# Optimization experiments

Hardware: AMD Instinct MI355X
Metric: run time of the kernel (lower is better)

Reference implementation:

```python
import jax, jax.numpy as jnp
import numpy as np

N = 50000      # nodes
E = 800000     # edges
D_IN = 512     # input feature dim
H1, C1 = 8, 8  # conv1: heads, per-head channels -> 64 concat
D_MID = H1 * C1
D_OUT = 64     # output_dim (classes)


def _lin(key, din, dout):
    # torch.nn.Linear default init: U(-1/sqrt(din), 1/sqrt(din))
    kw, kb = jax.random.split(key)
    s = 1.0 / np.sqrt(din)
    W = jax.random.uniform(kw, (din, dout), minval=-s, maxval=s, dtype=jnp.float32)
    b = jax.random.uniform(kb, (dout,), minval=-s, maxval=s, dtype=jnp.float32)
    return W, b


def setup_inputs() -> dict:
    key = jax.random.key(0)
    ks = jax.random.split(key, 10)
    x = jax.random.normal(ks[0], (N, D_IN), dtype=jnp.float32)
    edge_index = jax.random.randint(ks[1], (2, E), 0, N, dtype=jnp.int64)
    Wq1, bq1 = _lin(ks[2], D_IN, D_MID)
    Wk1, bk1 = _lin(ks[3], D_IN, D_MID)
    Wv1, bv1 = _lin(ks[4], D_IN, D_MID)
    Ws1, bs1 = _lin(ks[5], D_IN, D_MID)          # skip (concat=True -> heads*out)
    Wq2, bq2 = _lin(ks[6], D_MID, D_OUT)
    Wk2, bk2 = _lin(ks[7], D_MID, D_OUT)
    Wv2, bv2 = _lin(ks[8], D_MID, D_OUT)
    Ws2, bs2 = _lin(ks[9], D_MID, D_OUT)         # skip (concat=False -> out)
    return dict(x=x, edge_index=edge_index,
                Wq1=Wq1, bq1=bq1, Wk1=Wk1, bk1=bk1, Wv1=Wv1, bv1=bv1, Ws1=Ws1, bs1=bs1,
                Wq2=Wq2, bq2=bq2, Wk2=Wk2, bk2=bk2, Wv2=Wv2, bv2=bv2, Ws2=Ws2, bs2=bs2)


def transformer_conv(x, src, dst, Wq, bq, Wk, bk, Wv, bv, Ws, bs, heads, out_ch, concat):
    # PyG TransformerConv (edge_dim=None, beta=False, root_weight=True), eval mode
    n = x.shape[0]
    q = (x @ Wq + bq).reshape(n, heads, out_ch)
    k = (x @ Wk + bk).reshape(n, heads, out_ch)
    v = (x @ Wv + bv).reshape(n, heads, out_ch)
    # per-edge scaled dot-product attention logits [E, H]
    alpha = jnp.einsum('ehc,ehc->eh', q[dst], k[src]) / np.sqrt(out_ch)
    # scatter-softmax over incoming edges of each target node
    amax = jax.ops.segment_max(alpha, dst, num_segments=n)            # [N, H]
    ex = jnp.exp(alpha - amax[dst])
    denom = jax.ops.segment_sum(ex, dst, num_segments=n)              # [N, H]
    a = ex / (denom[dst] + 1e-16)                                     # [E, H]
    # weighted scatter-add of values
    out = jax.ops.segment_sum(a[:, :, None] * v[src], dst, num_segments=n)  # [N, H, C]
    out = out.reshape(n, heads * out_ch) if concat else out.mean(axis=1)
    return out + (x @ Ws + bs)  # root/skip connection


def reference(x, edge_index, Wq1, bq1, Wk1, bk1, Wv1, bv1, Ws1, bs1,
              Wq2, bq2, Wk2, bk2, Wv2, bv2, Ws2, bs2):
    src, dst = edge_index[0], edge_index[1]   # message flows j=src -> i=dst
    # dropout layers are no-ops in eval mode
    h = transformer_conv(x, src, dst, Wq1, bq1, Wk1, bk1, Wv1, bv1, Ws1, bs1, H1, C1, True)
    h = jax.nn.elu(h)
    h = transformer_conv(h, src, dst, Wq2, bq2, Wk2, bk2, Wv2, bv2, Ws2, bs2, 1, D_OUT, False)
    return jax.nn.log_softmax(h, axis=-1)
```

## Files before the change

kernel.cpp:

```cpp
#include <hip/hip_runtime.h>
#include <hip/hip_bf16.h>
#include <math.h>


typedef __attribute__((ext_vector_type(4))) float f32x4;
typedef __attribute__((ext_vector_type(8))) short bf16x8;
typedef __attribute__((ext_vector_type(8))) unsigned short u16x8;

__device__ inline unsigned short f2bf(float f) {
    union { float f; unsigned u; } v; v.f = f;
    unsigned r = (v.u + 0x7fffu + ((v.u >> 16) & 1u)) >> 16;
    return (unsigned short)r;
}
__device__ inline float bf2f(unsigned short u) {
    union { unsigned u; float f; } v; v.u = ((unsigned)u) << 16; return v.f;
}

#define NEGBIG (-1e30f)

__device__ inline void prep_panel(int i, int K,
                                  const float* __restrict__ W0, const float* __restrict__ b0,
                                  const float* __restrict__ W1, const float* __restrict__ b1,
                                  const float* __restrict__ W2, const float* __restrict__ b2,
                                  const float* __restrict__ W3, const float* __restrict__ b3,
                                  unsigned short* __restrict__ Btp, float* __restrict__ bias) {
    int tot = 4 * K * 64;
    if (i < tot) {
        int j    = i & 7;
        int lane = (i >> 3) & 63;
        int ni   = (i >> 9) & 3;
        int kk   = (i >> 11) & 1;
        int w    = (i >> 12) & 3;
        int ks   = i >> 14;
        int ncol = ni * 16 + (lane & 15);
        int k    = ks * 64 + kk * 32 + ((lane >> 4) << 3) + j;
        const float* W = (w == 0) ? W0 : (w == 1) ? W1 : (w == 2) ? W2 : W3;
        Btp[i] = f2bf(W[k * 64 + ncol]);
    }
    if (i < 256) {
        int which = i >> 6;
        const float* b = (which == 0) ? b0 : (which == 1) ? b1 : (which == 2) ? b2 : b3;
        bias[i] = b[i & 63];
    }
}

__global__ void setup_all(const float* __restrict__ Wq1, const float* __restrict__ bq1,
                          const float* __restrict__ Wk1, const float* __restrict__ bk1,
                          const float* __restrict__ Wv1, const float* __restrict__ bv1,
                          const float* __restrict__ Ws1, const float* __restrict__ bs1,
                          const float* __restrict__ Wq2, const float* __restrict__ bq2,
                          const float* __restrict__ Wk2, const float* __restrict__ bk2,
                          const float* __restrict__ Wv2, const float* __restrict__ bv2,
                          const float* __restrict__ Ws2, const float* __restrict__ bs2,
                          unsigned short* __restrict__ bt1, float* __restrict__ bias1,
                          unsigned short* __restrict__ bt2, float* __restrict__ bias2,
                          int* __restrict__ deg, int* __restrict__ cursor, int N) {
    const int b = blockIdx.x;
    const int tid = threadIdx.x;
    if (b < 512) {
        prep_panel(b * 256 + tid, 512, Wq1, bq1, Wk1, bk1, Wv1, bv1, Ws1, bs1, bt1, bias1);
    } else if (b < 512 + 64) {
        prep_panel((b - 512) * 256 + tid, 64, Wq2, bq2, Wk2, bk2, Wv2, bv2, Ws2, bs2, bt2, bias2);
    } else {
        int i = (b - 576) * 256 + tid;
        if (i < N) { deg[i] = 0; cursor[i] = 0; }
    }
}

template<int KSTEPS, bool ABF16>
__global__ __launch_bounds__(256) void gemm_mfma(const void* __restrict__ Av, int M,
                                                 const unsigned short* __restrict__ Bt,
                                                 const float* __restrict__ bias,
                                                 unsigned short* __restrict__ outbf) {
    constexpr int K = KSTEPS * 64;
    __shared__ unsigned short As[2][64][72];
    const int tid = threadIdx.x;
    const int lane = tid & 63;
    const int w = tid >> 6;
    const int node0 = blockIdx.x * 64;
    const int r16 = lane & 15, g = lane >> 4;

    f32x4 acc[4][4] = {};

    const int srow = tid >> 2;
    const int sc0 = (tid & 3) * 16;
    const int node = node0 + srow;
    const bool nvalid = node < M;

    float4 f0, f1, f2, f3;
    u16x8 a0, a1;

#define ISSUE_LOAD(KS)                                                                     \
    do {                                                                                   \
        if (ABF16) {                                                                       \
            a0 = (u16x8){}; a1 = (u16x8){};                                                \
            if (nvalid) {                                                                  \
                const u16x8* p = (const u16x8*)((const unsigned short*)Av +                \
                                  (size_t)node * K + (KS) * 64 + sc0);                     \
                a0 = p[0]; a1 = p[1];                                                      \
            }                                                                              \
        } else {                                                                           \
            f0 = make_float4(0.f, 0.f, 0.f, 0.f); f1 = f0; f2 = f0; f3 = f0;               \
            if (nvalid) {                                                                  \
                const float4* p = (const float4*)((const float*)Av +                       \
                                   (size_t)node * K + (KS) * 64 + sc0);                    \
                f0 = p[0]; f1 = p[1]; f2 = p[2]; f3 = p[3];                                \
            }                                                                              \
        }                                                                                  \
    } while (0)

#define WRITE_LDS(BUF)                                                                     \
    do {                                                                                   \
        unsigned short t[16];                                                              \
        if (ABF16) {                                                                       \
            _Pragma("unroll")                                                              \
            for (int j = 0; j < 8; ++j) { t[j] = a0[j]; t[8 + j] = a1[j]; }                \
        } else {                                                                           \
            t[0] = f2bf(f0.x); t[1] = f2bf(f0.y); t[2] = f2bf(f0.z); t[3] = f2bf(f0.w);    \
            t[4] = f2bf(f1.x); t[5] = f2bf(f1.y); t[6] = f2bf(f1.z); t[7] = f2bf(f1.w);    \
            t[8] = f2bf(f2.x); t[9] = f2bf(f2.y); t[10] = f2bf(f2.z); t[11] = f2bf(f2.w);  \
            t[12] = f2bf(f3.x); t[13] = f2bf(f3.y); t[14] = f2bf(f3.z); t[15] = f2bf(f3.w);\
        }                                                                                  \
        u16x8 w0, w1;                                                                      \
        _Pragma("unroll")                                                                  \
        for (int j = 0; j < 8; ++j) { w0[j] = t[j]; w1[j] = t[8 + j]; }                    \
        *(u16x8*)&As[BUF][srow][sc0] = w0;                                                 \
        *(u16x8*)&As[BUF][srow][sc0 + 8] = w1;                                             \
    } while (0)

    ISSUE_LOAD(0);
    WRITE_LDS(0);
    __syncthreads();

#pragma unroll
    for (int ks = 0; ks < KSTEPS; ++ks) {
        bf16x8 bfr[8];
#pragma unroll
        for (int kk = 0; kk < 2; ++kk)
#pragma unroll
            for (int ni = 0; ni < 4; ++ni)
                bfr[kk * 4 + ni] = *(const bf16x8*)&Bt[
                    ((size_t)(((ks * 4 + w) * 2 + kk) * 4 + ni) << 9) + (lane << 3)];
        if (ks + 1 < KSTEPS) ISSUE_LOAD(ks + 1);

#pragma unroll
        for (int kk = 0; kk < 2; ++kk) {
            bf16x8 afr[4];
#pragma unroll
            for (int mi = 0; mi < 4; ++mi)
                afr[mi] = *(const bf16x8*)&As[ks & 1][mi * 16 + r16][kk * 32 + g * 8];
#pragma unroll
            for (int ni = 0; ni < 4; ++ni)
#pragma unroll
                for (int mi = 0; mi < 4; ++mi)
                    acc[mi][ni] = __builtin_amdgcn_mfma_f32_16x16x32_bf16(
                        afr[mi], bfr[kk * 4 + ni], acc[mi][ni], 0, 0, 0);
        }

        if (ks + 1 < KSTEPS) WRITE_LDS((ks + 1) & 1);
        __syncthreads();
    }
#undef ISSUE_LOAD
#undef WRITE_LDS

#pragma unroll
    for (int mi = 0; mi < 4; ++mi) {
#pragma unroll
        for (int r = 0; r < 4; ++r) {
            int row = node0 + mi * 16 + g * 4 + r;
            if (row < M) {
                size_t o = (size_t)row * 256 + w * 64;
#pragma unroll
                for (int ni = 0; ni < 4; ++ni)
                    outbf[o + ni * 16 + r16] =
                        f2bf(acc[mi][ni][r] + bias[w * 64 + ni * 16 + r16]);
            }
        }
    }
}

__global__ void hist_deg(const int* __restrict__ dst, int E, int N, int* __restrict__ deg) {
    int e = blockIdx.x * 256 + threadIdx.x;
    if (e >= E) return;
    int d = dst[e];
    if ((unsigned)d < (unsigned)N) atomicAdd(&deg[d], 1);
}

__global__ __launch_bounds__(256) void scan_blk_k(const int* __restrict__ deg, int N,
                                                  int* __restrict__ rowptr,
                                                  int* __restrict__ blk_sums) {
    __shared__ int wsum[4];
    const int t = threadIdx.x;
    const int base = blockIdx.x * 1024 + t * 4;
    int d0 = 0, d1 = 0, d2 = 0, d3 = 0;
    if (base + 3 < N) {
        int4 v = *(const int4*)&deg[base];
        d0 = v.x; d1 = v.y; d2 = v.z; d3 = v.w;
    } else {
        if (base < N)     d0 = deg[base];
        if (base + 1 < N) d1 = deg[base + 1];
        if (base + 2 < N) d2 = deg[base + 2];
    }
    int s = d0 + d1 + d2 + d3;
    int incl = s;
    const int lane = t & 63, w = t >> 6;
#pragma unroll
    for (int off = 1; off < 64; off <<= 1) {
        int v = __shfl_up(incl, off, 64);
        if (lane >= off) incl += v;
    }
    if (lane == 63) wsum[w] = incl;
    __syncthreads();
    int woff = 0;
    if (w > 0) woff += wsum[0];
    if (w > 1) woff += wsum[1];
    if (w > 2) woff += wsum[2];
    int excl = woff + incl - s;
    if (base < N)     rowptr[base]     = excl;
    if (base + 1 < N) rowptr[base + 1] = excl + d0;
    if (base + 2 < N) rowptr[base + 2] = excl + d0 + d1;
    if (base + 3 < N) rowptr[base + 3] = excl + d0 + d1 + d2;
    if (t == 255) blk_sums[blockIdx.x] = woff + incl;
}

__global__ __launch_bounds__(64) void scan_top_k(const int* __restrict__ blk_sums,
                                                 int* __restrict__ blk_off, int nblk,
                                                 int* __restrict__ rowptrN) {
    const int lane = threadIdx.x;
    int carry = 0;
    for (int b = 0; b < nblk; b += 64) {
        int idx = b + lane;
        int v = (idx < nblk) ? blk_sums[idx] : 0;
        int incl = v;
#pragma unroll
        for (int off = 1; off < 64; off <<= 1) {
            int u = __shfl_up(incl, off, 64);
            if (lane >= off) incl += u;
        }
        if (idx < nblk) blk_off[idx] = carry + incl - v;
        carry += __shfl(incl, 63, 64);
    }
    if (lane == 0) *rowptrN = carry;
}

__global__ __launch_bounds__(256) void scan_add_k(int* __restrict__ rowptr,
                                                  const int* __restrict__ blk_off, int N) {
    const int base = blockIdx.x * 1024 + threadIdx.x * 4;
    const int off = blk_off[blockIdx.x];
    if (base + 3 < N) {
        int4 v = *(int4*)&rowptr[base];
        v.x += off; v.y += off; v.z += off; v.w += off;
        *(int4*)&rowptr[base] = v;
    } else {
        for (int i = 0; i < 4; ++i)
            if (base + i < N) rowptr[base + i] += off;
    }
}

__global__ void scatter_edges(const int* __restrict__ src, const int* __restrict__ dst,
                              int E, int N,
                              const int* __restrict__ rowptr, int* __restrict__ cursor,
                              int* __restrict__ csr_src) {
    int e = blockIdx.x * 256 + threadIdx.x;
    if (e >= E) return;
    int d = dst[e];
    if ((unsigned)d >= (unsigned)N) return;
    int slot = rowptr[d] + atomicAdd(&cursor[d], 1);
    if ((unsigned)slot < (unsigned)E) csr_src[slot] = src[e];
}

__global__ __launch_bounds__(256) void attn1(const unsigned short* __restrict__ qbf,
                                             const int* __restrict__ rowptr,
                                             const int* __restrict__ csr_src,
                                             unsigned short* __restrict__ h1bf, int N) {
    int node = blockIdx.x * 4 + (threadIdx.x >> 6);
    if (node >= N) return;
    const int lane = threadIdx.x & 63;
    const int g = lane >> 3, h = lane & 7;

    float q[8];
    {
        u16x8 qv = *(const u16x8*)(qbf + (size_t)node * 256 + h * 8);
#pragma unroll
        for (int i = 0; i < 8; ++i) q[i] = bf2f(qv[i]);
    }

    const float SC = 1.44269504f * 0.35355339059327373f;
    float m = NEGBIG, l = 0.f;
    float a[8] = {};

    const int beg = rowptr[node], end = rowptr[node + 1];
    const int nt = (end - beg + 15) >> 4;

    for (int t = 0; t < nt; ++t) {
        int i0 = beg + t * 16 + g;
        int i1 = i0 + 8;
        bool v0 = i0 < end, v1 = i1 < end;
        int s0 = csr_src[v0 ? i0 : beg];
        int s1 = csr_src[v1 ? i1 : beg];
        s0 = ((unsigned)s0 < (unsigned)N) ? s0 : 0;
        s1 = ((unsigned)s1 < (unsigned)N) ? s1 : 0;
        const unsigned short* kb0 = qbf + (size_t)s0 * 256 + 64 + h * 8;
        const unsigned short* kb1 = qbf + (size_t)s1 * 256 + 64 + h * 8;
        u16x8 ku0 = *(const u16x8*)kb0;
        u16x8 vu0 = *(const u16x8*)(kb0 + 64);
        u16x8 ku1 = *(const u16x8*)kb1;
        u16x8 vu1 = *(const u16x8*)(kb1 + 64);
        float p0 = 0.f, p1 = 0.f;
#pragma unroll
        for (int i = 0; i < 8; ++i) { p0 += q[i] * bf2f(ku0[i]); p1 += q[i] * bf2f(ku1[i]); }
        float x0 = v0 ? (p0 * SC) : NEGBIG;
        float x1 = v1 ? (p1 * SC) : NEGBIG;
        float mnew = fmaxf(m, fmaxf(x0, x1));
        float corr = exp2f(m - mnew);
        float w0 = v0 ? exp2f(x0 - mnew) : 0.f;
        float w1 = v1 ? exp2f(x1 - mnew) : 0.f;
        l = l * corr + w0 + w1;
#pragma unroll
        for (int i = 0; i < 8; ++i)
            a[i] = a[i] * corr + w0 * bf2f(vu0[i]) + w1 * bf2f(vu1[i]);
        m = mnew;
    }

#pragma unroll
    for (int off = 8; off <= 32; off <<= 1) {
        float mo = __shfl_xor(m, off, 64);
        float lo = __shfl_xor(l, off, 64);
        float mn = fmaxf(m, mo);
        float s1 = exp2f(m - mn);
        float s2 = exp2f(mo - mn);
        l = l * s1 + lo * s2;
#pragma unroll
        for (int i = 0; i < 8; ++i) {
            float ao = __shfl_xor(a[i], off, 64);
            a[i] = a[i] * s1 + ao * s2;
        }
        m = mn;
    }

    if (g == 0) {
        float inv = 1.f / (l + 1e-16f);
        u16x8 sv = *(const u16x8*)(qbf + (size_t)node * 256 + 192 + h * 8);
        u16x8 o;
#pragma unroll
        for (int i = 0; i < 8; ++i) {
            float t = a[i] * inv + bf2f(sv[i]);
            t = (t > 0.f) ? t : expm1f(t);
            o[i] = f2bf(t);
        }
        *(u16x8*)(h1bf + (size_t)node * 64 + h * 8) = o;
    }
}

__global__ __launch_bounds__(256) void attn2(const unsigned short* __restrict__ qbf,
                                             const int* __restrict__ rowptr,
                                             const int* __restrict__ csr_src,
                                             float* __restrict__ out, int N) {
    int node = blockIdx.x * 4 + (threadIdx.x >> 6);
    if (node >= N) return;
    const int lane = threadIdx.x & 63;
    const int g = lane >> 4, j = lane & 15;

    float qx, qy, qz, qw;
    {
        ushort4 qv = *(const ushort4*)(qbf + (size_t)node * 256 + j * 4);
        qx = bf2f(qv.x); qy = bf2f(qv.y); qz = bf2f(qv.z); qw = bf2f(qv.w);
    }
    const float SC = 1.44269504f * 0.125f;
    float m = NEGBIG, l = 0.f;
    float4 acc = make_float4(0.f, 0.f, 0.f, 0.f);

    const int beg = rowptr[node], end = rowptr[node + 1];
    const int nt = (end - beg + 7) >> 3;

    for (int t = 0; t < nt; ++t) {
        int i0 = beg + t * 8 + g;
        int i1 = i0 + 4;
        bool v0 = i0 < end, v1 = i1 < end;
        int s0 = csr_src[v0 ? i0 : beg];
        int s1 = csr_src[v1 ? i1 : beg];
        s0 = ((unsigned)s0 < (unsigned)N) ? s0 : 0;
        s1 = ((unsigned)s1 < (unsigned)N) ? s1 : 0;
        const unsigned short* kb0 = qbf + (size_t)s0 * 256 + 64 + j * 4;
        const unsigned short* kb1 = qbf + (size_t)s1 * 256 + 64 + j * 4;
        ushort4 ku0 = *(const ushort4*)kb0;
        ushort4 vu0 = *(const ushort4*)(kb0 + 64);
        ushort4 ku1 = *(const ushort4*)kb1;
        ushort4 vu1 = *(const ushort4*)(kb1 + 64);
        float p0 = qx * bf2f(ku0.x) + qy * bf2f(ku0.y)
                 + qz * bf2f(ku0.z) + qw * bf2f(ku0.w);
        float p1 = qx * bf2f(ku1.x) + qy * bf2f(ku1.y)
                 + qz * bf2f(ku1.z) + qw * bf2f(ku1.w);
#pragma unroll
        for (int mask = 1; mask <= 8; mask <<= 1) {
            p0 += __shfl_xor(p0, mask, 64);
            p1 += __shfl_xor(p1, mask, 64);
        }
        float x0 = v0 ? (p0 * SC) : NEGBIG;
        float x1 = v1 ? (p1 * SC) : NEGBIG;
        float mnew = fmaxf(m, fmaxf(x0, x1));
        float corr = exp2f(m - mnew);
        float w0 = v0 ? exp2f(x0 - mnew) : 0.f;
        float w1 = v1 ? exp2f(x1 - mnew) : 0.f;
        l = l * corr + w0 + w1;
        acc.x = acc.x * corr + w0 * bf2f(vu0.x) + w1 * bf2f(vu1.x);
        acc.y = acc.y * corr + w0 * bf2f(vu0.y) + w1 * bf2f(vu1.y);
        acc.z = acc.z * corr + w0 * bf2f(vu0.z) + w1 * bf2f(vu1.z);
        acc.w = acc.w * corr + w0 * bf2f(vu0.w) + w1 * bf2f(vu1.w);
        m = mnew;
    }

#pragma unroll
    for (int off = 16; off <= 32; off <<= 1) {
        float mo = __shfl_xor(m, off, 64);
        float lo = __shfl_xor(l, off, 64);
        float ax = __shfl_xor(acc.x, off, 64);
        float ay = __shfl_xor(acc.y, off, 64);
        float az = __shfl_xor(acc.z, off, 64);
        float aw = __shfl_xor(acc.w, off, 64);
        float mn = fmaxf(m, mo);
        float s1 = exp2f(m - mn);
        float s2 = exp2f(mo - mn);
        l = l * s1 + lo * s2;
        acc.x = acc.x * s1 + ax * s2;
        acc.y = acc.y * s1 + ay * s2;
        acc.z = acc.z * s1 + az * s2;
        acc.w = acc.w * s1 + aw * s2;
        m = mn;
    }

    float inv = 1.f / (l + 1e-16f);
    ushort4 sv = *(const ushort4*)(qbf + (size_t)node * 256 + 192 + j * 4);
    float4 t4;
    t4.x = acc.x * inv + bf2f(sv.x);
    t4.y = acc.y * inv + bf2f(sv.y);
    t4.z = acc.z * inv + bf2f(sv.z);
    t4.w = acc.w * inv + bf2f(sv.w);

    float mx = fmaxf(fmaxf(t4.x, t4.y), fmaxf(t4.z, t4.w));
#pragma unroll
    for (int off = 1; off <= 8; off <<= 1) mx = fmaxf(mx, __shfl_xor(mx, off, 64));
    float es = expf(t4.x - mx) + expf(t4.y - mx) + expf(t4.z - mx) + expf(t4.w - mx);
#pragma unroll
    for (int off = 1; off <= 8; off <<= 1) es += __shfl_xor(es, off, 64);
    float ls = logf(es);
    if (g == 0) {
        float4 o;
        o.x = (t4.x - mx) - ls;
        o.y = (t4.y - mx) - ls;
        o.z = (t4.z - mx) - ls;
        o.w = (t4.w - mx) - ls;
        *(float4*)&out[(size_t)node * 64 + j * 4] = o;
    }
}

extern "C" void kernel_launch(void* const* d_in, const int* in_sizes, int n_in,
                              void* d_out, int out_size, void* d_ws, size_t ws_size,
                              hipStream_t stream) {
    const int N = in_sizes[0] / 512;
    const int E = in_sizes[1] / 2;
    const float* x   = (const float*)d_in[0];
    const int*   ei  = (const int*)d_in[1];
    const int* src = ei;
    const int* dst = ei + E;
    const float *Wq1 = (const float*)d_in[2],  *bq1 = (const float*)d_in[3];
    const float *Wk1 = (const float*)d_in[4],  *bk1 = (const float*)d_in[5];
    const float *Wv1 = (const float*)d_in[6],  *bv1 = (const float*)d_in[7];
    const float *Ws1 = (const float*)d_in[8],  *bs1 = (const float*)d_in[9];
    const float *Wq2 = (const float*)d_in[10], *bq2 = (const float*)d_in[11];
    const float *Wk2 = (const float*)d_in[12], *bk2 = (const float*)d_in[13];
    const float *Wv2 = (const float*)d_in[14], *bv2 = (const float*)d_in[15];
    const float *Ws2 = (const float*)d_in[16], *bs2 = (const float*)d_in[17];

    auto align16 = [](size_t v) { return (v + 15) & ~(size_t)15; };

    const int nblk = (N + 1023) / 1024;

    float* ws = (float*)d_ws;
    const size_t OFF_QBF  = 0;
    const size_t OFF_H1B  = align16(OFF_QBF  + (size_t)N * 128);
    const size_t OFF_BT1  = align16(OFF_H1B  + (size_t)N * 32);
    const size_t OFF_BT2  = align16(OFF_BT1  + 65536);
    const size_t OFF_BI1  = align16(OFF_BT2  + 8192);
    const size_t OFF_BI2  = align16(OFF_BI1  + 256);
    const size_t OFF_ROWP = align16(OFF_BI2  + 256);
    const size_t OFF_DEG  = align16(OFF_ROWP + (size_t)N + 1);
    const size_t OFF_CUR  = align16(OFF_DEG  + (size_t)N);
    const size_t OFF_CSRC = align16(OFF_CUR  + (size_t)N);
    const size_t OFF_BSUM = align16(OFF_CSRC + (size_t)E);
    const size_t OFF_BOFF = align16(OFF_BSUM + (size_t)nblk);
    const size_t TOTAL    = align16(OFF_BOFF + (size_t)nblk);
    if (ws_size < TOTAL * sizeof(float)) return;

    unsigned short* qbf  = (unsigned short*)(ws + OFF_QBF);
    unsigned short* h1bf = (unsigned short*)(ws + OFF_H1B);
    unsigned short* bt1  = (unsigned short*)(ws + OFF_BT1);
    unsigned short* bt2  = (unsigned short*)(ws + OFF_BT2);
    float* bias1 = ws + OFF_BI1;
    float* bias2 = ws + OFF_BI2;
    int* rowptr  = (int*)(ws + OFF_ROWP);
    int* deg     = (int*)(ws + OFF_DEG);
    int* cursor  = (int*)(ws + OFF_CUR);
    int* csr_src = (int*)(ws + OFF_CSRC);
    int* blk_sums = (int*)(ws + OFF_BSUM);
    int* blk_off  = (int*)(ws + OFF_BOFF);
    float* out   = (float*)d_out;

    const int gBlocks = (N + 63) / 64;
    const int nBlocks4 = (N + 3) / 4;
    const int zBlocks = (N + 255) / 256;

    setup_all<<<512 + 64 + zBlocks, 256, 0, stream>>>(
        Wq1, bq1, Wk1, bk1, Wv1, bv1, Ws1, bs1,
        Wq2, bq2, Wk2, bk2, Wv2, bv2, Ws2, bs2,
        bt1, bias1, bt2, bias2, deg, cursor, N);

    hist_deg<<<(E + 255) / 256, 256, 0, stream>>>(dst, E, N, deg);
    scan_blk_k<<<nblk, 256, 0, stream>>>(deg, N, rowptr, blk_sums);
    scan_top_k<<<1, 64, 0, stream>>>(blk_sums, blk_off, nblk, &rowptr[N]);
    scan_add_k<<<nblk, 256, 0, stream>>>(rowptr, blk_off, N);
    scatter_edges<<<(E + 255) / 256, 256, 0, stream>>>(src, dst, E, N, rowptr, cursor, csr_src);

    gemm_mfma<8, false><<<gBlocks, 256, 0, stream>>>(x, N, bt1, bias1, qbf);
    attn1<<<nBlocks4, 256, 0, stream>>>(qbf, rowptr, csr_src, h1bf, N);

    gemm_mfma<1, true><<<gBlocks, 256, 0, stream>>>(h1bf, N, bt2, bias2, qbf);
    attn2<<<nBlocks4, 256, 0, stream>>>(qbf, rowptr, csr_src, out, N);
}
```

Before: 227.5 us.

## Fuse degree histogram into layer-1 GEMM launch and drop separate cursor array

Merges the edge-degree histogram into the first projection GEMM as extra blocks of one grid, so the memory-bound GEMM and the atomic histogram run concurrently in a single launch. The histogram is vectorised to read four destinations per thread. The per-node cursor array is replaced by a copy of the row pointers that scatter atomically increments, which removes one zeroing pass and one load per edge. This adds register and LDS pressure considerations to a mixed-role kernel, and GEMM blocks may contend with atomic traffic.

```diff
diff --git a/kernel.cpp b/kernel.cpp
--- a/kernel.cpp
+++ b/kernel.cpp
@@ -54,7 +54,7 @@
                           const float* __restrict__ Ws2, const float* __restrict__ bs2,
                           unsigned short* __restrict__ bt1, float* __restrict__ bias1,
                           unsigned short* __restrict__ bt2, float* __restrict__ bias2,
-                          int* __restrict__ deg, int* __restrict__ cursor, int N) {
+                          int* __restrict__ deg, int N) {
     const int b = blockIdx.x;
     const int tid = threadIdx.x;
     if (b < 512) {
@@ -63,21 +63,21 @@
         prep_panel((b - 512) * 256 + tid, 64, Wq2, bq2, Wk2, bk2, Wv2, bv2, Ws2, bs2, bt2, bias2);
     } else {
         int i = (b - 576) * 256 + tid;
-        if (i < N) { deg[i] = 0; cursor[i] = 0; }
+        if (i < N) deg[i] = 0;
     }
 }
 
 template<int KSTEPS, bool ABF16>
-__global__ __launch_bounds__(256) void gemm_mfma(const void* __restrict__ Av, int M,
-                                                 const unsigned short* __restrict__ Bt,
-                                                 const float* __restrict__ bias,
-                                                 unsigned short* __restrict__ outbf) {
+__device__ void gemm_body(const void* __restrict__ Av, int M,
+                          const unsigned short* __restrict__ Bt,
+                          const float* __restrict__ bias,
+                          unsigned short* __restrict__ outbf, int blk) {
     constexpr int K = KSTEPS * 64;
     __shared__ unsigned short As[2][64][72];
     const int tid = threadIdx.x;
     const int lane = tid & 63;
     const int w = tid >> 6;
-    const int node0 = blockIdx.x * 64;
+    const int node0 = blk * 64;
     const int r16 = lane & 15, g = lane >> 4;
 
     f32x4 acc[4][4] = {};
@@ -179,11 +179,40 @@
     }
 }
 
-__global__ void hist_deg(const int* __restrict__ dst, int E, int N, int* __restrict__ deg) {
-    int e = blockIdx.x * 256 + threadIdx.x;
-    if (e >= E) return;
-    int d = dst[e];
-    if ((unsigned)d < (unsigned)N) atomicAdd(&deg[d], 1);
+template<int KSTEPS, bool ABF16>
+__global__ __launch_bounds__(256) void gemm_mfma(const void* __restrict__ Av, int M,
+                                                 const unsigned short* __restrict__ Bt,
+                                                 const float* __restrict__ bias,
+                                                 unsigned short* __restrict__ outbf) {
+    gemm_body<KSTEPS, ABF16>(Av, M, Bt, bias, outbf, blockIdx.x);
+}
+
+__global__ __launch_bounds__(256) void gemm1_hist(const float* __restrict__ x, int M,
+                                                  const unsigned short* __restrict__ Bt,
+                                                  const float* __restrict__ bias,
+                                                  unsigned short* __restrict__ outbf,
+                                                  const int* __restrict__ dst, int E, int N,
+                                                  int* __restrict__ deg, int gB) {
+    if (blockIdx.x < gB) {
+        gemm_body<8, false>(x, M, Bt, bias, outbf, blockIdx.x);
+    } else {
+        int base = ((blockIdx.x - gB) * 256 + threadIdx.x) * 4;
+        if (base + 3 < E) {
+            int4 d4 = *(const int4*)&dst[base];
+            if ((unsigned)d4.x < (unsigned)N) atomicAdd(&deg[d4.x], 1);
+            if ((unsigned)d4.y < (unsigned)N) atomicAdd(&deg[d4.y], 1);
+            if ((unsigned)d4.z < (unsigned)N) atomicAdd(&deg[d4.z], 1);
+            if ((unsigned)d4.w < (unsigned)N) atomicAdd(&deg[d4.w], 1);
+        } else {
+            for (int i = 0; i < 4; ++i) {
+                int e = base + i;
+                if (e < E) {
+                    int d = dst[e];
+                    if ((unsigned)d < (unsigned)N) atomicAdd(&deg[d], 1);
+                }
+            }
+        }
+    }
 }
 
 __global__ __launch_bounds__(256) void scan_blk_k(const int* __restrict__ deg, int N,
@@ -244,6 +273,7 @@
 }
 
 __global__ __launch_bounds__(256) void scan_add_k(int* __restrict__ rowptr,
+                                                  int* __restrict__ rowptr2,
                                                   const int* __restrict__ blk_off, int N) {
     const int base = blockIdx.x * 1024 + threadIdx.x * 4;
     const int off = blk_off[blockIdx.x];
@@ -251,21 +281,25 @@
         int4 v = *(int4*)&rowptr[base];
         v.x += off; v.y += off; v.z += off; v.w += off;
         *(int4*)&rowptr[base] = v;
+        *(int4*)&rowptr2[base] = v;
     } else {
         for (int i = 0; i < 4; ++i)
-            if (base + i < N) rowptr[base + i] += off;
+            if (base + i < N) {
+                int v = rowptr[base + i] + off;
+                rowptr[base + i] = v;
+                rowptr2[base + i] = v;
+            }
     }
 }
 
 __global__ void scatter_edges(const int* __restrict__ src, const int* __restrict__ dst,
                               int E, int N,
-                              const int* __restrict__ rowptr, int* __restrict__ cursor,
-                              int* __restrict__ csr_src) {
+                              int* __restrict__ rowptr2, int* __restrict__ csr_src) {
     int e = blockIdx.x * 256 + threadIdx.x;
     if (e >= E) return;
     int d = dst[e];
     if ((unsigned)d >= (unsigned)N) return;
-    int slot = rowptr[d] + atomicAdd(&cursor[d], 1);
+    int slot = atomicAdd(&rowptr2[d], 1);
     if ((unsigned)slot < (unsigned)E) csr_src[slot] = src[e];
 }
 
@@ -485,8 +519,8 @@
     const size_t OFF_BI2  = align16(OFF_BI1  + 256);
     const size_t OFF_ROWP = align16(OFF_BI2  + 256);
     const size_t OFF_DEG  = align16(OFF_ROWP + (size_t)N + 1);
-    const size_t OFF_CUR  = align16(OFF_DEG  + (size_t)N);
-    const size_t OFF_CSRC = align16(OFF_CUR  + (size_t)N);
+    const size_t OFF_ROW2 = align16(OFF_DEG  + (size_t)N);
+    const size_t OFF_CSRC = align16(OFF_ROW2 + (size_t)N);
     const size_t OFF_BSUM = align16(OFF_CSRC + (size_t)E);
     const size_t OFF_BOFF = align16(OFF_BSUM + (size_t)nblk);
     const size_t TOTAL    = align16(OFF_BOFF + (size_t)nblk);
@@ -500,7 +534,7 @@
     float* bias2 = ws + OFF_BI2;
     int* rowptr  = (int*)(ws + OFF_ROWP);
     int* deg     = (int*)(ws + OFF_DEG);
-    int* cursor  = (int*)(ws + OFF_CUR);
+    int* rowptr2 = (int*)(ws + OFF_ROW2);
     int* csr_src = (int*)(ws + OFF_CSRC);
     int* blk_sums = (int*)(ws + OFF_BSUM);
     int* blk_off  = (int*)(ws + OFF_BOFF);
@@ -509,19 +543,21 @@
     const int gBlocks = (N + 63) / 64;
     const int nBlocks4 = (N + 3) / 4;
     const int zBlocks = (N + 255) / 256;
+    const int histBlocks = (E / 4 + 255) / 256;
 
     setup_all<<<512 + 64 + zBlocks, 256, 0, stream>>>(
         Wq1, bq1, Wk1, bk1, Wv1, bv1, Ws1, bs1,
         Wq2, bq2, Wk2, bk2, Wv2, bv2, Ws2, bs2,
-        bt1, bias1, bt2, bias2, deg, cursor, N);
-
-    hist_deg<<<(E + 255) / 256, 256, 0, stream>>>(dst, E, N, deg);
+        bt1, bias1, bt2, bias2, deg, N);
+
+    gemm1_hist<<<gBlocks + histBlocks, 256, 0, stream>>>(
+        x, N, bt1, bias1, qbf, dst, E, N, deg, gBlocks);
+
     scan_blk_k<<<nblk, 256, 0, stream>>>(deg, N, rowptr, blk_sums);
     scan_top_k<<<1, 64, 0, stream>>>(blk_sums, blk_off, nblk, &rowptr[N]);
-    scan_add_k<<<nblk, 256, 0, stream>>>(rowptr, blk_off, N);
-    scatter_edges<<<(E + 255) / 256, 256, 0, stream>>>(src, dst, E, N, rowptr, cursor, csr_src);
-
-    gemm_mfma<8, false><<<gBlocks, 256, 0, stream>>>(x, N, bt1, bias1, qbf);
+    scan_add_k<<<nblk, 256, 0, stream>>>(rowptr, rowptr2, blk_off, N);
+    scatter_edges<<<(E + 255) / 256, 256, 0, stream>>>(src, dst, E, N, rowptr2, csr_src);
+
     attn1<<<nBlocks4, 256, 0, stream>>>(qbf, rowptr, csr_src, h1bf, N);
 
     gemm_mfma<1, true><<<gBlocks, 256, 0, stream>>>(h1bf, N, bt2, bias2, qbf);
```

Result: faster. 217.5 us, median of 3 (-4.4%).
